# Kernel optimization log

Measured on AMD Instinct MI355X. Metric: run time of the kernel, lower is better.

The kernel has to match this reference:

```python
import jax, jax.numpy as jnp
import numpy as np

MAX_DEPTH = 8
LMBDA = 0.1
OUTPUT_DIM = 128


def setup_inputs() -> dict:
    key = jax.random.key(0)
    k1, k2, k3, k4, k5, k6 = jax.random.split(key, 6)
    B, D, C = 8192, 2048, OUTPUT_DIM
    n_inner = 2 ** MAX_DEPTH - 1  # 255 inner nodes, BFS order
    n_leaf = 2 ** MAX_DEPTH       # 256 leaves
    x = jax.random.normal(k1, (B, D), dtype=jnp.float32)
    target = jax.random.randint(k2, (B,), 0, C)
    # small scale so sigmoid gates are not saturated (log(pen), log(1-pen) finite)
    W = jax.random.normal(k3, (n_inner, D), dtype=jnp.float32) * 0.02
    b = jax.random.normal(k4, (n_inner,), dtype=jnp.float32) * 0.02
    beta = jax.random.normal(k5, (n_inner,), dtype=jnp.float32)
    leaf_params = jax.random.normal(k6, (n_leaf, C), dtype=jnp.float32)
    return {"x": x, "target": target, "W": W, "b": b, "beta": beta,
            "leaf_params": leaf_params}


def reference(x, target, W, b, beta, leaf_params):
    B = x.shape[0]
    C = leaf_params.shape[1]
    y = jax.nn.one_hot(target, C, dtype=x.dtype)  # target_onehot

    # All inner-node gates as one batched GEMM: p[b,i] = sigmoid(beta_i*(x@w_i+b_i))
    p = jax.nn.sigmoid(beta[None, :] * (x @ W.T + b[None, :]))  # [B, n_inner]

    # Level-by-level path probability propagation (BFS node order).
    path = jnp.ones((B, 1), x.dtype)
    penalties = []  # per-level [2^d] node penalties
    start = 0
    for d in range(MAX_DEPTH):
        n = 2 ** d
        p_lvl = p[:, start:start + n]                      # [B, 2^d]
        pen = jnp.sum(p_lvl * path, axis=0) / jnp.sum(path, axis=0)
        penalties.append(pen)
        # left child gets path*(1-p), right gets path*p; interleave -> next level
        path = jnp.stack([path * (1.0 - p_lvl), path * p_lvl], axis=-1).reshape(B, 2 * n)
        start += n
    # path: [B, n_leaf] leaf path probabilities (left-to-right order)

    Q = jax.nn.softmax(leaf_params, axis=-1)               # [n_leaf, C]
    TQ = y @ jnp.log(Q).T                                  # [B, n_leaf], y . log Q per leaf
    loss = jnp.mean(jnp.sum(path * TQ, axis=1))

    # Penalty C: only inner nodes whose children are NOT leaves contribute
    # (original get_penalty drops depth==max_depth nodes), depths 1..max_depth-1.
    Cpen = jnp.asarray(0.0, x.dtype)
    for d in range(MAX_DEPTH - 1):
        lam = LMBDA * 2.0 ** (-(d + 1))
        pen = penalties[d]
        Cpen = Cpen - lam * 0.5 * jnp.sum(jnp.log(pen) + jnp.log(1.0 - pen))

    total = -loss + Cpen

    # output: Q of the max-path-prob leaf per sample
    leaf_idx = jnp.argmax(path, axis=1)                    # [B]
    output = Q[leaf_idx]                                   # [B, C]
    return total, output
```

## Files before the change

kernel.cpp:

```cpp
#include <hip/hip_runtime.h>
#include <hip/hip_bf16.h>
#include <hip/hip_fp16.h>
#include <stdint.h>

#define B_SIZE 8192
#define D_SIZE 2048
#define C_SIZE 128
#define N_INNER 255
#define N_LEAF 256
#define NPAD 256
#define NBLK_PATH 512

typedef _Float16 half8 __attribute__((ext_vector_type(8)));
typedef __fp16 pk16x2 __attribute__((ext_vector_type(2)));
typedef float f32x4 __attribute__((ext_vector_type(4)));
typedef unsigned short u16;

__device__ inline uint32_t pkh(float a, float b) {
    pk16x2 h = __builtin_amdgcn_cvt_pkrtz(a, b);
    return __builtin_bit_cast(uint32_t, h);
}
__device__ inline void split4(const float4 v, uint2& hi, uint2& lo) {
    pk16x2 a01 = __builtin_amdgcn_cvt_pkrtz(v.x, v.y);
    pk16x2 a23 = __builtin_amdgcn_cvt_pkrtz(v.z, v.w);
    float r0 = v.x - (float)a01[0];
    float r1 = v.y - (float)a01[1];
    float r2 = v.z - (float)a23[0];
    float r3 = v.w - (float)a23[1];
    hi = make_uint2(__builtin_bit_cast(uint32_t, a01), __builtin_bit_cast(uint32_t, a23));
    lo = make_uint2(pkh(r0, r1), pkh(r2, r3));
}

__global__ __launch_bounds__(256) void prep_kernel(
    const float* __restrict__ Wsrc, u16* __restrict__ Wh, u16* __restrict__ Wl,
    const float* __restrict__ lp, float* __restrict__ Q, float* __restrict__ logQt)
{
    int bid = blockIdx.x;
    int t = threadIdx.x;
    if (bid < 256) {
        int row = bid;
        int k = t * 8;
        uint2 h0, l0, h1, l1;
        if (row < N_INNER) {
            float4 v0 = *(const float4*)(Wsrc + (size_t)row * D_SIZE + k);
            float4 v1 = *(const float4*)(Wsrc + (size_t)row * D_SIZE + k + 4);
            split4(v0, h0, l0); split4(v1, h1, l1);
        } else {
            h0 = l0 = h1 = l1 = make_uint2(0u, 0u);
        }
        *(uint2*)&Wh[(size_t)row * D_SIZE + k]     = h0;
        *(uint2*)&Wh[(size_t)row * D_SIZE + k + 4] = h1;
        *(uint2*)&Wl[(size_t)row * D_SIZE + k]     = l0;
        *(uint2*)&Wl[(size_t)row * D_SIZE + k + 4] = l1;
    } else {
        int row = bid - 256;
        __shared__ float red[128];
        float v = 0.f;
        if (t < 128) { v = lp[row * C_SIZE + t]; red[t] = v; }
        __syncthreads();
        for (int s = 64; s > 0; s >>= 1) { if (t < s) red[t] = fmaxf(red[t], red[t + s]); __syncthreads(); }
        float mx = red[0]; __syncthreads();
        float e = 0.f;
        if (t < 128) { e = expf(v - mx); red[t] = e; }
        __syncthreads();
        for (int s = 64; s > 0; s >>= 1) { if (t < s) red[t] += red[t + s]; __syncthreads(); }
        float sum = red[0];
        if (t < 128) {
            Q[row * C_SIZE + t] = e / sum;
            logQt[(size_t)t * N_LEAF + row] = (v - mx) - logf(sum);
        }
    }
}

#define GBM 64
#define GBK 32
#define LDKA 40

template<int KS>
__global__ __launch_bounds__(256, 2) void gemm_mfma(
    const float* __restrict__ x, const u16* __restrict__ Wh, const u16* __restrict__ Wl,
    float* __restrict__ zp)
{
    constexpr int KCH = D_SIZE / KS;
    constexpr int KIT = KCH / GBK;

    __shared__ __align__(16) u16 sAh[4][GBM * LDKA];
    __shared__ __align__(16) u16 sAl[4][GBM * LDKA];

    const int t = threadIdx.x;
    const int lane = t & 63, w = t >> 6;
    const int lr = lane & 15, lq = lane >> 4;
    const int kz = blockIdx.x & (KS - 1);
    const int mi = blockIdx.x / KS;
    const int m0 = mi * GBM;
    const int kb0 = kz * KCH;

    f32x4 acc[4][4];
    #pragma unroll
    for (int mt = 0; mt < 4; ++mt)
        #pragma unroll
        for (int nt = 0; nt < 4; ++nt) acc[mt][nt] = (f32x4){0.f, 0.f, 0.f, 0.f};

    float4 av_c[8];
    #pragma unroll
    for (int i = 0; i < 8; ++i) {
        int idx = i * 64 + lane;
        int row = idx >> 3, ch = idx & 7;
        av_c[i] = *(const float4*)(x + (size_t)(m0 + row) * D_SIZE + kb0 + ch * 4);
    }
    half8 bh[4], bl[4];
    #pragma unroll
    for (int nt = 0; nt < 4; ++nt) {
        int row = w * 64 + nt * 16 + lr;
        bh[nt] = *(const half8*)(Wh + (size_t)row * D_SIZE + kb0 + lq * 8);
        bl[nt] = *(const half8*)(Wl + (size_t)row * D_SIZE + kb0 + lq * 8);
    }

    #pragma unroll
    for (int kt = 0; kt < KIT; ++kt) {
        const int kb = kb0 + kt * GBK;
        half8 nbh[4], nbl[4];
        if (kt + 1 < KIT) {
            #pragma unroll
            for (int nt = 0; nt < 4; ++nt) {
                int row = w * 64 + nt * 16 + lr;
                nbh[nt] = *(const half8*)(Wh + (size_t)row * D_SIZE + kb + GBK + lq * 8);
                nbl[nt] = *(const half8*)(Wl + (size_t)row * D_SIZE + kb + GBK + lq * 8);
            }
        }
        float4 av_n[8];
        if (kt + 1 < KIT) {
            #pragma unroll
            for (int i = 0; i < 8; ++i) {
                int idx = i * 64 + lane;
                int row = idx >> 3, ch = idx & 7;
                av_n[i] = *(const float4*)(x + (size_t)(m0 + row) * D_SIZE + kb + GBK + ch * 4);
            }
        }
        #pragma unroll
        for (int i = 0; i < 8; ++i) {
            int idx = i * 64 + lane;
            int row = idx >> 3, ch = idx & 7;
            uint2 hi, lo; split4(av_c[i], hi, lo);
            *(uint2*)&sAh[w][row * LDKA + ch * 4] = hi;
            *(uint2*)&sAl[w][row * LDKA + ch * 4] = lo;
        }
        asm volatile("s_waitcnt lgkmcnt(0)" ::: "memory");
        half8 ah[4], al[4];
        #pragma unroll
        for (int mt = 0; mt < 4; ++mt) {
            int off = (mt * 16 + lr) * LDKA + lq * 8;
            ah[mt] = *(const half8*)&sAh[w][off];
            al[mt] = *(const half8*)&sAl[w][off];
        }
        #pragma unroll
        for (int mt = 0; mt < 4; ++mt)
            #pragma unroll
            for (int nt = 0; nt < 4; ++nt) {
                acc[mt][nt] = __builtin_amdgcn_mfma_f32_16x16x32_f16(ah[mt], bh[nt], acc[mt][nt], 0, 0, 0);
                acc[mt][nt] = __builtin_amdgcn_mfma_f32_16x16x32_f16(ah[mt], bl[nt], acc[mt][nt], 0, 0, 0);
                acc[mt][nt] = __builtin_amdgcn_mfma_f32_16x16x32_f16(al[mt], bh[nt], acc[mt][nt], 0, 0, 0);
            }
        if (kt + 1 < KIT) {
            #pragma unroll
            for (int i = 0; i < 8; ++i) av_c[i] = av_n[i];
            #pragma unroll
            for (int nt = 0; nt < 4; ++nt) { bh[nt] = nbh[nt]; bl[nt] = nbl[nt]; }
        }
    }

    float* zout = zp + (size_t)kz * B_SIZE * NPAD;
    #pragma unroll
    for (int mt = 0; mt < 4; ++mt) {
        #pragma unroll
        for (int nt = 0; nt < 4; ++nt) {
            int gn = w * 64 + nt * 16 + lr;
            #pragma unroll
            for (int r = 0; r < 4; ++r) {
                int gm = m0 + mt * 16 + lq * 4 + r;
                zout[(size_t)gm * NPAD + gn] = acc[mt][nt][r];
            }
        }
    }
}

template<int KS>
__global__ __launch_bounds__(256) void path_kernel(
    const float* __restrict__ z, const int* __restrict__ target,
    const float* __restrict__ bvec, const float* __restrict__ beta,
    const float* __restrict__ Q, const float* __restrict__ logQt,
    float* __restrict__ partial, float* __restrict__ out)
{
    __shared__ float pbuf[4][256];
    __shared__ float s_num[128], s_den[128], s_loss;
    const int t = threadIdx.x, w = t >> 6, lane = t & 63;
    const int c0 = lane * 4;
    float pnum[4] = {0.f, 0.f, 0.f, 0.f};
    float pden[4] = {0.f, 0.f, 0.f, 0.f};
    float loss = 0.f;

    if (t < 128) s_num[t] = 0.f;
    else s_den[t - 128] = 0.f;
    if (t == 0) s_loss = 0.f;
    __syncthreads();

    float bet[4], bia[4];
    #pragma unroll
    for (int j = 0; j < 4; ++j) {
        int c = c0 + j;
        bet[j] = (c < N_INNER) ? beta[c] : 0.f;
        bia[j] = (c < N_INNER) ? bvec[c] : 0.f;
    }

    for (int i = 0; i < 4; ++i) {
        int r = blockIdx.x * 16 + w * 4 + i;
        float4 s = make_float4(0.f, 0.f, 0.f, 0.f);
        #pragma unroll
        for (int p = 0; p < KS; ++p) {
            float4 v = *(const float4*)(z + ((size_t)p * B_SIZE + r) * NPAD + c0);
            s.x += v.x; s.y += v.y; s.z += v.z; s.w += v.w;
        }
        float zv[4] = {s.x, s.y, s.z, s.w};
        float pv[4];
        #pragma unroll
        for (int j = 0; j < 4; ++j) {
            int c = c0 + j;
            pv[j] = (c < N_INNER) ? 1.f / (1.f + expf(-bet[j] * (zv[j] + bia[j]))) : 0.f;
        }
        *(float4*)&pbuf[w][c0] = make_float4(pv[0], pv[1], pv[2], pv[3]);
        asm volatile("s_waitcnt lgkmcnt(0)" ::: "memory");

        int tg = target[r];
        float4 lq4 = *(const float4*)(logQt + (size_t)tg * N_LEAF + c0);
        float lqa[4] = {lq4.x, lq4.y, lq4.z, lq4.w};
        float lsum = 0.f, bestV = -1.f;
        int bestI = 0;
        #pragma unroll
        for (int j = 0; j < 4; ++j) {
            int leaf = c0 + j;
            float pl = 1.f;
            #pragma unroll
            for (int d = 0; d < 8; ++d) {
                int node = (1 << d) - 1 + (leaf >> (8 - d));
                int bit = (leaf >> (7 - d)) & 1;
                float pvn = pbuf[w][node];
                pl *= bit ? pvn : (1.f - pvn);
            }
            lsum += pl * lqa[j];
            if (pl > bestV) { bestV = pl; bestI = leaf; }
        }
        if (lane < 32) {
            #pragma unroll
            for (int j = 0; j < 4; ++j) {
                int c = c0 + j;
                if (c < 127) {
                    int h = c + 1; int d = 31 - __clz(h);
                    float pp = 1.f;
                    for (int e = 0; e < d; ++e) {
                        int ha = h >> (d - e);
                        int bit = (h >> (d - 1 - e)) & 1;
                        float pvn = pbuf[w][ha - 1];
                        pp *= bit ? pvn : (1.f - pvn);
                    }
                    pnum[j] += pbuf[w][c] * pp;
                    pden[j] += pp;
                }
            }
        }
        #pragma unroll
        for (int m = 1; m < 64; m <<= 1) {
            lsum += __shfl_xor(lsum, m, 64);
            float ov = __shfl_xor(bestV, m, 64);
            int   oi = __shfl_xor(bestI, m, 64);
            if (ov > bestV || (ov == bestV && oi < bestI)) { bestV = ov; bestI = oi; }
        }
        loss += lsum;
        out[1 + (size_t)r * C_SIZE + lane]      = Q[bestI * C_SIZE + lane];
        out[1 + (size_t)r * C_SIZE + lane + 64] = Q[bestI * C_SIZE + lane + 64];
        asm volatile("" ::: "memory");
    }

    if (lane < 32) {
        #pragma unroll
        for (int j = 0; j < 4; ++j) {
            int c = c0 + j;
            if (c < 127) {
                atomicAdd(&s_num[c], pnum[j]);
                atomicAdd(&s_den[c], pden[j]);
            }
        }
    }
    if (lane == 0) atomicAdd(&s_loss, loss);
    __syncthreads();
    float* rec = partial + (size_t)blockIdx.x * 256;
    if (t < 127)        rec[t] = s_num[t];
    else if (t == 127)  rec[127] = s_loss;
    else if (t < 255)   rec[t] = s_den[t - 128];
    else                rec[255] = 0.f;
}

__global__ __launch_bounds__(1024) void reduce_kernel(
    const float* __restrict__ partial, float* __restrict__ out)
{
    __shared__ float part[4][256];
    __shared__ float s[256];
    __shared__ float red[128];
    const int t = threadIdx.x;
    const int col = t & 255, seg = t >> 8;
    const int base = seg * (NBLK_PATH / 4);
    float a0 = 0.f, a1 = 0.f, a2 = 0.f, a3 = 0.f;
    for (int r = 0; r < NBLK_PATH / 4; r += 4) {
        a0 += partial[(size_t)(base + r + 0) * 256 + col];
        a1 += partial[(size_t)(base + r + 1) * 256 + col];
        a2 += partial[(size_t)(base + r + 2) * 256 + col];
        a3 += partial[(size_t)(base + r + 3) * 256 + col];
    }
    part[seg][col] = (a0 + a1) + (a2 + a3);
    __syncthreads();
    if (t < 256) s[t] = (part[0][t] + part[1][t]) + (part[2][t] + part[3][t]);
    __syncthreads();
    float term = 0.f;
    if (t < 127) {
        int d = 31 - __clz(t + 1);
        float lam = 0.1f * exp2f(-(float)(d + 1));
        float pen = s[t] / s[128 + t];
        term = lam * 0.5f * (logf(pen) + logf(1.f - pen));
    }
    if (t < 128) { red[t] = term; }
    __syncthreads();
    for (int sh = 64; sh > 0; sh >>= 1) { if (t < sh) red[t] += red[t + sh]; __syncthreads(); }
    if (t == 0) out[0] = -(s[127] / (float)B_SIZE) - red[0];
}

extern "C" void kernel_launch(void* const* d_in, const int* in_sizes, int n_in,
                              void* d_out, int out_size, void* d_ws, size_t ws_size,
                              hipStream_t stream)
{
    const float* x    = (const float*)d_in[0];
    const int*   tgt  = (const int*)d_in[1];
    const float* W    = (const float*)d_in[2];
    const float* b    = (const float*)d_in[3];
    const float* beta = (const float*)d_in[4];
    const float* lp   = (const float*)d_in[5];
    float* out = (float*)d_out;

    const size_t tail_bytes = (size_t)N_LEAF * C_SIZE * 4 + (size_t)C_SIZE * N_LEAF * 4
                            + 2 * (size_t)N_LEAF * D_SIZE * 2 + (size_t)NBLK_PATH * 256 * 4;
    const size_t need8 = (size_t)8 * B_SIZE * NPAD * 4 + tail_bytes;
    const bool use8 = (ws_size >= need8);
    const int KS = use8 ? 8 : 4;

    float* z     = (float*)d_ws;
    float* Q     = z + (size_t)KS * B_SIZE * NPAD;
    float* logQt = Q + (size_t)N_LEAF * C_SIZE;
    u16*   Wh    = (u16*)(logQt + (size_t)C_SIZE * N_LEAF);
    u16*   Wl    = Wh + (size_t)N_LEAF * D_SIZE;
    float* partial = (float*)(Wl + (size_t)N_LEAF * D_SIZE);

    prep_kernel<<<512, 256, 0, stream>>>(W, Wh, Wl, lp, Q, logQt);

    if (use8) {
        gemm_mfma<8><<<128 * 8, 256, 0, stream>>>(x, Wh, Wl, z);
        path_kernel<8><<<NBLK_PATH, 256, 0, stream>>>(z, tgt, b, beta, Q, logQt, partial, out);
    } else {
        gemm_mfma<4><<<128 * 4, 256, 0, stream>>>(x, Wh, Wl, z);
        path_kernel<4><<<NBLK_PATH, 256, 0, stream>>>(z, tgt, b, beta, Q, logQt, partial, out);
    }

    reduce_kernel<<<1, 1024, 0, stream>>>(partial, out);
}
```

Measured before the change: 185.8 us.

## Fuse gate GEMM with path kernel, dropping split-K z buffer

Replaces the split-K GEMM that wrote partial logits to a large global z buffer, plus the separate path kernel, with one kernel. Each block computes the full-K logits for 16 rows, stages them in shared memory, and runs the path/loss/argmax logic in place. Leaf path products now reuse a shared 6-level prefix per lane instead of walking 8 levels per leaf. This removes the global z write/read and one launch. In exchange, every block streams the whole hi/lo W matrix with only 16 rows of reuse, and each wave reloads the same x tile, so L2 traffic on W rises sharply and the long sequential K loop may limit throughput.

```diff
diff --git a/kernel.cpp b/kernel.cpp
--- a/kernel.cpp
+++ b/kernel.cpp
@@ -8,7 +8,6 @@
 #define C_SIZE 128
 #define N_INNER 255
 #define N_LEAF 256
-#define NPAD 256
 #define NBLK_PATH 512
 
 typedef _Float16 half8 __attribute__((ext_vector_type(8)));
@@ -72,73 +71,70 @@
     }
 }
 
-#define GBM 64
-#define GBK 32
+#define FBM 16
+#define FBK 32
+#define FKIT (D_SIZE / FBK)
 #define LDKA 40
 
-template<int KS>
-__global__ __launch_bounds__(256, 2) void gemm_mfma(
+__global__ __launch_bounds__(256, 2) void gemm_path(
     const float* __restrict__ x, const u16* __restrict__ Wh, const u16* __restrict__ Wl,
-    float* __restrict__ zp)
+    const int* __restrict__ target, const float* __restrict__ bvec, const float* __restrict__ beta,
+    const float* __restrict__ Q, const float* __restrict__ logQt,
+    float* __restrict__ partial, float* __restrict__ out)
 {
-    constexpr int KCH = D_SIZE / KS;
-    constexpr int KIT = KCH / GBK;
-
-    __shared__ __align__(16) u16 sAh[4][GBM * LDKA];
-    __shared__ __align__(16) u16 sAl[4][GBM * LDKA];
+    __shared__ __align__(16) u16 sAh[4][FBM * LDKA];
+    __shared__ __align__(16) u16 sAl[4][FBM * LDKA];
+    __shared__ float zbuf[FBM][256];
+    __shared__ float s_num[128], s_den[128], s_loss;
 
     const int t = threadIdx.x;
     const int lane = t & 63, w = t >> 6;
     const int lr = lane & 15, lq = lane >> 4;
-    const int kz = blockIdx.x & (KS - 1);
-    const int mi = blockIdx.x / KS;
-    const int m0 = mi * GBM;
-    const int kb0 = kz * KCH;
-
-    f32x4 acc[4][4];
-    #pragma unroll
-    for (int mt = 0; mt < 4; ++mt)
-        #pragma unroll
-        for (int nt = 0; nt < 4; ++nt) acc[mt][nt] = (f32x4){0.f, 0.f, 0.f, 0.f};
-
-    float4 av_c[8];
-    #pragma unroll
-    for (int i = 0; i < 8; ++i) {
+    const int m0 = blockIdx.x * FBM;
+
+    if (t < 128) s_num[t] = 0.f;
+    else s_den[t - 128] = 0.f;
+    if (t == 0) s_loss = 0.f;
+
+    f32x4 acc[4];
+    #pragma unroll
+    for (int nt = 0; nt < 4; ++nt) acc[nt] = (f32x4){0.f, 0.f, 0.f, 0.f};
+
+    float4 av_c[2];
+    #pragma unroll
+    for (int i = 0; i < 2; ++i) {
         int idx = i * 64 + lane;
         int row = idx >> 3, ch = idx & 7;
-        av_c[i] = *(const float4*)(x + (size_t)(m0 + row) * D_SIZE + kb0 + ch * 4);
+        av_c[i] = *(const float4*)(x + (size_t)(m0 + row) * D_SIZE + ch * 4);
     }
     half8 bh[4], bl[4];
     #pragma unroll
     for (int nt = 0; nt < 4; ++nt) {
         int row = w * 64 + nt * 16 + lr;
-        bh[nt] = *(const half8*)(Wh + (size_t)row * D_SIZE + kb0 + lq * 8);
-        bl[nt] = *(const half8*)(Wl + (size_t)row * D_SIZE + kb0 + lq * 8);
-    }
-
-    #pragma unroll
-    for (int kt = 0; kt < KIT; ++kt) {
-        const int kb = kb0 + kt * GBK;
+        bh[nt] = *(const half8*)(Wh + (size_t)row * D_SIZE + lq * 8);
+        bl[nt] = *(const half8*)(Wl + (size_t)row * D_SIZE + lq * 8);
+    }
+
+    #pragma unroll 4
+    for (int kt = 0; kt < FKIT; ++kt) {
+        const int kb = kt * FBK;
+        const int kn = (kt + 1 < FKIT) ? kb + FBK : kb;
         half8 nbh[4], nbl[4];
-        if (kt + 1 < KIT) {
-            #pragma unroll
-            for (int nt = 0; nt < 4; ++nt) {
-                int row = w * 64 + nt * 16 + lr;
-                nbh[nt] = *(const half8*)(Wh + (size_t)row * D_SIZE + kb + GBK + lq * 8);
-                nbl[nt] = *(const half8*)(Wl + (size_t)row * D_SIZE + kb + GBK + lq * 8);
-            }
-        }
-        float4 av_n[8];
-        if (kt + 1 < KIT) {
-            #pragma unroll
-            for (int i = 0; i < 8; ++i) {
-                int idx = i * 64 + lane;
-                int row = idx >> 3, ch = idx & 7;
-                av_n[i] = *(const float4*)(x + (size_t)(m0 + row) * D_SIZE + kb + GBK + ch * 4);
-            }
-        }
-        #pragma unroll
-        for (int i = 0; i < 8; ++i) {
+        #pragma unroll
+        for (int nt = 0; nt < 4; ++nt) {
+            int row = w * 64 + nt * 16 + lr;
+            nbh[nt] = *(const half8*)(Wh + (size_t)row * D_SIZE + kn + lq * 8);
+            nbl[nt] = *(const half8*)(Wl + (size_t)row * D_SIZE + kn + lq * 8);
+        }
+        float4 av_n[2];
+        #pragma unroll
+        for (int i = 0; i < 2; ++i) {
+            int idx = i * 64 + lane;
+            int row = idx >> 3, ch = idx & 7;
+            av_n[i] = *(const float4*)(x + (size_t)(m0 + row) * D_SIZE + kn + ch * 4);
+        }
+        #pragma unroll
+        for (int i = 0; i < 2; ++i) {
             int idx = i * 64 + lane;
             int row = idx >> 3, ch = idx & 7;
             uint2 hi, lo; split4(av_c[i], hi, lo);
@@ -146,64 +142,30 @@
             *(uint2*)&sAl[w][row * LDKA + ch * 4] = lo;
         }
         asm volatile("s_waitcnt lgkmcnt(0)" ::: "memory");
-        half8 ah[4], al[4];
-        #pragma unroll
-        for (int mt = 0; mt < 4; ++mt) {
-            int off = (mt * 16 + lr) * LDKA + lq * 8;
-            ah[mt] = *(const half8*)&sAh[w][off];
-            al[mt] = *(const half8*)&sAl[w][off];
-        }
-        #pragma unroll
-        for (int mt = 0; mt < 4; ++mt)
-            #pragma unroll
-            for (int nt = 0; nt < 4; ++nt) {
-                acc[mt][nt] = __builtin_amdgcn_mfma_f32_16x16x32_f16(ah[mt], bh[nt], acc[mt][nt], 0, 0, 0);
-                acc[mt][nt] = __builtin_amdgcn_mfma_f32_16x16x32_f16(ah[mt], bl[nt], acc[mt][nt], 0, 0, 0);
-                acc[mt][nt] = __builtin_amdgcn_mfma_f32_16x16x32_f16(al[mt], bh[nt], acc[mt][nt], 0, 0, 0);
-            }
-        if (kt + 1 < KIT) {
-            #pragma unroll
-            for (int i = 0; i < 8; ++i) av_c[i] = av_n[i];
-            #pragma unroll
-            for (int nt = 0; nt < 4; ++nt) { bh[nt] = nbh[nt]; bl[nt] = nbl[nt]; }
-        }
-    }
-
-    float* zout = zp + (size_t)kz * B_SIZE * NPAD;
-    #pragma unroll
-    for (int mt = 0; mt < 4; ++mt) {
+        half8 ah = *(const half8*)&sAh[w][lr * LDKA + lq * 8];
+        half8 al = *(const half8*)&sAl[w][lr * LDKA + lq * 8];
         #pragma unroll
         for (int nt = 0; nt < 4; ++nt) {
-            int gn = w * 64 + nt * 16 + lr;
-            #pragma unroll
-            for (int r = 0; r < 4; ++r) {
-                int gm = m0 + mt * 16 + lq * 4 + r;
-                zout[(size_t)gm * NPAD + gn] = acc[mt][nt][r];
-            }
-        }
-    }
-}
-
-template<int KS>
-__global__ __launch_bounds__(256) void path_kernel(
-    const float* __restrict__ z, const int* __restrict__ target,
-    const float* __restrict__ bvec, const float* __restrict__ beta,
-    const float* __restrict__ Q, const float* __restrict__ logQt,
-    float* __restrict__ partial, float* __restrict__ out)
-{
-    __shared__ float pbuf[4][256];
-    __shared__ float s_num[128], s_den[128], s_loss;
-    const int t = threadIdx.x, w = t >> 6, lane = t & 63;
+            acc[nt] = __builtin_amdgcn_mfma_f32_16x16x32_f16(ah, bh[nt], acc[nt], 0, 0, 0);
+            acc[nt] = __builtin_amdgcn_mfma_f32_16x16x32_f16(ah, bl[nt], acc[nt], 0, 0, 0);
+            acc[nt] = __builtin_amdgcn_mfma_f32_16x16x32_f16(al, bh[nt], acc[nt], 0, 0, 0);
+        }
+        #pragma unroll
+        for (int i = 0; i < 2; ++i) av_c[i] = av_n[i];
+        #pragma unroll
+        for (int nt = 0; nt < 4; ++nt) { bh[nt] = nbh[nt]; bl[nt] = nbl[nt]; }
+    }
+
+    #pragma unroll
+    for (int nt = 0; nt < 4; ++nt) {
+        int gn = w * 64 + nt * 16 + lr;
+        #pragma unroll
+        for (int r = 0; r < 4; ++r)
+            zbuf[lq * 4 + r][gn] = acc[nt][r];
+    }
+    __syncthreads();
+
     const int c0 = lane * 4;
-    float pnum[4] = {0.f, 0.f, 0.f, 0.f};
-    float pden[4] = {0.f, 0.f, 0.f, 0.f};
-    float loss = 0.f;
-
-    if (t < 128) s_num[t] = 0.f;
-    else s_den[t - 128] = 0.f;
-    if (t == 0) s_loss = 0.f;
-    __syncthreads();
-
     float bet[4], bia[4];
     #pragma unroll
     for (int j = 0; j < 4; ++j) {
@@ -211,43 +173,60 @@
         bet[j] = (c < N_INNER) ? beta[c] : 0.f;
         bia[j] = (c < N_INNER) ? bvec[c] : 0.f;
     }
-
+    int tg[4];
+    #pragma unroll
+    for (int i = 0; i < 4; ++i) tg[i] = target[m0 + w * 4 + i];
+
+    #pragma unroll
     for (int i = 0; i < 4; ++i) {
-        int r = blockIdx.x * 16 + w * 4 + i;
-        float4 s = make_float4(0.f, 0.f, 0.f, 0.f);
-        #pragma unroll
-        for (int p = 0; p < KS; ++p) {
-            float4 v = *(const float4*)(z + ((size_t)p * B_SIZE + r) * NPAD + c0);
-            s.x += v.x; s.y += v.y; s.z += v.z; s.w += v.w;
-        }
-        float zv[4] = {s.x, s.y, s.z, s.w};
+        int row = w * 4 + i;
+        float4 zv4 = *(const float4*)&zbuf[row][c0];
+        float zv[4] = {zv4.x, zv4.y, zv4.z, zv4.w};
         float pv[4];
         #pragma unroll
         for (int j = 0; j < 4; ++j) {
             int c = c0 + j;
             pv[j] = (c < N_INNER) ? 1.f / (1.f + expf(-bet[j] * (zv[j] + bia[j]))) : 0.f;
         }
-        *(float4*)&pbuf[w][c0] = make_float4(pv[0], pv[1], pv[2], pv[3]);
-        asm volatile("s_waitcnt lgkmcnt(0)" ::: "memory");
-
-        int tg = target[r];
-        float4 lq4 = *(const float4*)(logQt + (size_t)tg * N_LEAF + c0);
-        float lqa[4] = {lq4.x, lq4.y, lq4.z, lq4.w};
+        *(float4*)&zbuf[row][c0] = make_float4(pv[0], pv[1], pv[2], pv[3]);
+    }
+    float4 lqv[4];
+    #pragma unroll
+    for (int i = 0; i < 4; ++i)
+        lqv[i] = *(const float4*)(logQt + (size_t)tg[i] * N_LEAF + c0);
+    asm volatile("s_waitcnt lgkmcnt(0)" ::: "memory");
+
+    float pnum[4] = {0.f, 0.f, 0.f, 0.f};
+    float pden[4] = {0.f, 0.f, 0.f, 0.f};
+    float loss = 0.f;
+
+    #pragma unroll
+    for (int i = 0; i < 4; ++i) {
+        const float* pb = zbuf[w * 4 + i];
+        const int r = m0 + w * 4 + i;
+        float lqa[4] = {lqv[i].x, lqv[i].y, lqv[i].z, lqv[i].w};
+
+        float P = 1.f;
+        #pragma unroll
+        for (int d = 0; d < 6; ++d) {
+            int node = (1 << d) - 1 + (c0 >> (8 - d));
+            int bit = (c0 >> (7 - d)) & 1;
+            float pvn = pb[node];
+            P *= bit ? pvn : (1.f - pvn);
+        }
+        float p6  = pb[63 + lane];
+        float p7a = pb[127 + 2 * lane];
+        float p7b = pb[127 + 2 * lane + 1];
         float lsum = 0.f, bestV = -1.f;
         int bestI = 0;
         #pragma unroll
         for (int j = 0; j < 4; ++j) {
-            int leaf = c0 + j;
-            float pl = 1.f;
-            #pragma unroll
-            for (int d = 0; d < 8; ++d) {
-                int node = (1 << d) - 1 + (leaf >> (8 - d));
-                int bit = (leaf >> (7 - d)) & 1;
-                float pvn = pbuf[w][node];
-                pl *= bit ? pvn : (1.f - pvn);
-            }
+            float t6 = (j & 2) ? p6 : (1.f - p6);
+            float p7 = (j & 2) ? p7b : p7a;
+            float t7 = (j & 1) ? p7 : (1.f - p7);
+            float pl = (P * t6) * t7;
             lsum += pl * lqa[j];
-            if (pl > bestV) { bestV = pl; bestI = leaf; }
+            if (pl > bestV) { bestV = pl; bestI = c0 + j; }
         }
         if (lane < 32) {
             #pragma unroll
@@ -259,10 +238,10 @@
                     for (int e = 0; e < d; ++e) {
                         int ha = h >> (d - e);
                         int bit = (h >> (d - 1 - e)) & 1;
-                        float pvn = pbuf[w][ha - 1];
+                        float pvn = pb[ha - 1];
                         pp *= bit ? pvn : (1.f - pvn);
                     }
-                    pnum[j] += pbuf[w][c] * pp;
+                    pnum[j] += pb[c] * pp;
                     pden[j] += pp;
                 }
             }
@@ -277,7 +256,6 @@
         loss += lsum;
         out[1 + (size_t)r * C_SIZE + lane]      = Q[bestI * C_SIZE + lane];
         out[1 + (size_t)r * C_SIZE + lane + 64] = Q[bestI * C_SIZE + lane + 64];
-        asm volatile("" ::: "memory");
     }
 
     if (lane < 32) {
@@ -344,28 +322,15 @@
     const float* lp   = (const float*)d_in[5];
     float* out = (float*)d_out;
 
-    const size_t tail_bytes = (size_t)N_LEAF * C_SIZE * 4 + (size_t)C_SIZE * N_LEAF * 4
-                            + 2 * (size_t)N_LEAF * D_SIZE * 2 + (size_t)NBLK_PATH * 256 * 4;
-    const size_t need8 = (size_t)8 * B_SIZE * NPAD * 4 + tail_bytes;
-    const bool use8 = (ws_size >= need8);
-    const int KS = use8 ? 8 : 4;
-
-    float* z     = (float*)d_ws;
-    float* Q     = z + (size_t)KS * B_SIZE * NPAD;
-    float* logQt = Q + (size_t)N_LEAF * C_SIZE;
-    u16*   Wh    = (u16*)(logQt + (size_t)C_SIZE * N_LEAF);
-    u16*   Wl    = Wh + (size_t)N_LEAF * D_SIZE;
-    float* partial = (float*)(Wl + (size_t)N_LEAF * D_SIZE);
+    u16*   Wh      = (u16*)d_ws;
+    u16*   Wl      = Wh + (size_t)N_LEAF * D_SIZE;
+    float* Q       = (float*)(Wl + (size_t)N_LEAF * D_SIZE);
+    float* logQt   = Q + (size_t)N_LEAF * C_SIZE;
+    float* partial = logQt + (size_t)C_SIZE * N_LEAF;
 
     prep_kernel<<<512, 256, 0, stream>>>(W, Wh, Wl, lp, Q, logQt);
 
-    if (use8) {
-        gemm_mfma<8><<<128 * 8, 256, 0, stream>>>(x, Wh, Wl, z);
-        path_kernel<8><<<NBLK_PATH, 256, 0, stream>>>(z, tgt, b, beta, Q, logQt, partial, out);
-    } else {
-        gemm_mfma<4><<<128 * 4, 256, 0, stream>>>(x, Wh, Wl, z);
-        path_kernel<4><<<NBLK_PATH, 256, 0, stream>>>(z, tgt, b, beta, Q, logQt, partial, out);
-    }
+    gemm_path<<<512, 256, 0, stream>>>(x, Wh, Wl, tgt, b, beta, Q, logQt, partial, out);
 
     reduce_kernel<<<1, 1024, 0, stream>>>(partial, out);
 }
```

New measurement: 244.6 us. 31.7% more time.
